# Kernel optimization log

Hardware: AMD Instinct MI355X
Metric: run time of the kernel (lower is better)

## Reference

```python
import jax, jax.numpy as jnp
import numpy as np

EPS_NORM = 1e-12   # F.normalize eps (denominator clamp)
EPS_PD = 1e-6      # F.pairwise_distance eps (added to the difference)
MARGIN = 0.3

B, D = 8192, 512


def setup_inputs() -> dict:
    key = jax.random.key(0)
    x = jax.random.normal(key, (B, D * 2), dtype=jnp.float32).reshape(B, 2, D)
    return {"x": x}


def reference(x):
    # x: [B, 2, D]  (anchor, positive)
    a = x[:, 0, :]
    p = x[:, 1, :]
    a = a / jnp.maximum(jnp.linalg.norm(a, axis=1, keepdims=True), EPS_NORM)
    p = p / jnp.maximum(jnp.linalg.norm(p, axis=1, keepdims=True), EPS_NORM)
    b, d = a.shape

    # output[i, j] = -||a_i - p_j + EPS_PD||^2, expanded so the BxB matrix
    # comes from one GEMM instead of a [B, D, B] broadcasted difference.
    sa2 = jnp.sum(a * a, axis=1)               # [B]
    sp2 = jnp.sum(p * p, axis=1)               # [B]
    dot = a @ p.T                              # [B, B]
    sa = jnp.sum(a, axis=1)                    # [B]
    sp = jnp.sum(p, axis=1)                    # [B]
    d2 = (sa2[:, None] + sp2[None, :] - 2.0 * dot
          + 2.0 * EPS_PD * (sa[:, None] - sp[None, :]) + d * (EPS_PD * EPS_PD))
    sim = -d2                                  # [B, B] similarity (detached in torch)

    # mineHardNegative with hard_rank=0, hard_prob=1: top-1 of descending sort
    # after removing the self index -> argmax over the row with diag masked.
    sim = jnp.where(jnp.eye(b, dtype=bool), -jnp.inf, sim)
    negidx = jnp.argmax(sim, axis=1)           # [B] int
    n = p[negidx]                              # hard negatives, [B, D]

    pos_d = jnp.linalg.norm(a - p + EPS_PD, axis=1)
    neg_d = jnp.linalg.norm(a - n + EPS_PD, axis=1)
    nloss = jnp.mean(jax.nn.relu(pos_d ** 2 - neg_d ** 2 + MARGIN))
    return nloss
```

## Files before the change

kernel.cpp:

```cpp
#include <hip/hip_runtime.h>
#include <stdint.h>
#include <math.h>

#define Bn 8192
#define Dn 512
#define EPSN 1e-12f
#define EPSP 1e-6f
#define MARG 0.3f

#define BM 128
#define BN 128
#define BKB 64
#define KT (Dn / BKB)
#define NCT (Bn / BN)
#define QS 256.0f
#define ISQ (2.0f / 65536.0f)

typedef int   int4v __attribute__((ext_vector_type(4)));
typedef float f32x4 __attribute__((ext_vector_type(4)));

__device__ __forceinline__ void async16(const void* g, void* l) {
    __builtin_amdgcn_global_load_lds(
        (const __attribute__((address_space(1))) void*)g,
        (__attribute__((address_space(3))) void*)l,
        16, 0, 0);
}

__device__ __forceinline__ unsigned long long packSI(float s, int idx) {
    union { float f; unsigned u; } c; c.f = s;
    const unsigned key = (c.u & 0x80000000u) ? ~c.u : (c.u | 0x80000000u);
    return ((unsigned long long)key << 32) | (unsigned)(~idx);
}
__device__ __forceinline__ float unpackS(unsigned long long p) {
    unsigned key = (unsigned)(p >> 32);
    union { unsigned u; float f; } c;
    c.u = (key & 0x80000000u) ? (key ^ 0x80000000u) : ~key;
    return c.f;
}

__global__ __launch_bounds__(256) void k_normalize(
    const float* __restrict__ x,
    uint8_t* __restrict__ a_i8, uint8_t* __restrict__ p_i8,
    float* __restrict__ cterm, float* __restrict__ rowconst,
    unsigned long long* __restrict__ rowmax)
{
    const int wave = threadIdx.x >> 6;
    const int lane = threadIdx.x & 63;
    const int i = blockIdx.x * 4 + wave;

    const float* srcA = x + (size_t)i * (2 * Dn) + lane * 8;
    const float* srcP = srcA + Dn;
    float4 a0 = ((const float4*)srcA)[0];
    float4 a1 = ((const float4*)srcA)[1];
    float4 p0 = ((const float4*)srcP)[0];
    float4 p1 = ((const float4*)srcP)[1];
    float va[8] = {a0.x, a0.y, a0.z, a0.w, a1.x, a1.y, a1.z, a1.w};
    float vp[8] = {p0.x, p0.y, p0.z, p0.w, p1.x, p1.y, p1.z, p1.w};

    float ssa = 0.f, ssp = 0.f;
#pragma unroll
    for (int j = 0; j < 8; ++j) { ssa += va[j] * va[j]; ssp += vp[j] * vp[j]; }
#pragma unroll
    for (int m = 1; m < 64; m <<= 1) {
        ssa += __shfl_xor(ssa, m);
        ssp += __shfl_xor(ssp, m);
    }
    const float sa = 1.0f / fmaxf(sqrtf(ssa), EPSN);
    const float sp = 1.0f / fmaxf(sqrtf(ssp), EPSN);

    float oa[8], op[8];
    float s1p = 0.f, s2p = 0.f, s1a = 0.f, s2a = 0.f, pos = 0.f;
#pragma unroll
    for (int j = 0; j < 8; ++j) {
        oa[j] = va[j] * sa;
        op[j] = vp[j] * sp;
        s1p += op[j]; s2p += op[j] * op[j];
        s1a += oa[j]; s2a += oa[j] * oa[j];
        const float u = oa[j] - op[j] + EPSP;
        pos += u * u;
    }

    uint64_t pka = 0, pkp = 0;
#pragma unroll
    for (int j = 0; j < 8; ++j) {
        int qa = (int)rintf(oa[j] * QS);
        int qp = (int)rintf(op[j] * QS);
        qa = qa > 127 ? 127 : (qa < -127 ? -127 : qa);
        qp = qp > 127 ? 127 : (qp < -127 ? -127 : qp);
        pka |= (uint64_t)(uint8_t)qa << (8 * j);
        pkp |= (uint64_t)(uint8_t)qp << (8 * j);
    }
    *(uint64_t*)(a_i8 + (size_t)i * Dn + lane * 8) = pka;
    *(uint64_t*)(p_i8 + (size_t)i * Dn + lane * 8) = pkp;

#pragma unroll
    for (int m = 1; m < 64; m <<= 1) {
        s1p += __shfl_xor(s1p, m);
        s2p += __shfl_xor(s2p, m);
        s1a += __shfl_xor(s1a, m);
        s2a += __shfl_xor(s2a, m);
        pos += __shfl_xor(pos, m);
    }
    if (lane == 0) {
        cterm[i] = -s2p + 2.0f * EPSP * s1p;
        rowconst[i] = pos - s2a - 2.0f * EPSP * s1a
                      - (float)Dn * EPSP * EPSP + MARG;
        rowmax[i] = 0ull;
    }
}

__global__ __launch_bounds__(256, 4) void k_gemm_argmax(
    const uint8_t* __restrict__ a_i8, const uint8_t* __restrict__ p_i8,
    const float* __restrict__ cterm,
    unsigned long long* __restrict__ rowmax)
{
    __shared__ uint8_t As[2][BM * BKB];
    __shared__ uint8_t Bs[2][BN * BKB];
    __shared__ unsigned long long rp[2][BM];

    const int t = threadIdx.x;
    const int wave = t >> 6;
    const int lane = t & 63;
    const int rowBase = blockIdx.y * BM;
    const int colBase = blockIdx.x * BN;

    const int q = lane >> 4;
    const int m16 = lane & 15;
    const int waveRow = (wave >> 1) * 64;
    const int waveCol = (wave & 1) * 64;

    const int r0 = t >> 2;
    const int g0 = (t & 3) ^ ((r0 >> 1) & 3);
    const int r1 = (256 + t) >> 2;
    const int g1 = ((256 + t) & 3) ^ ((r1 >> 1) & 3);
    const uint8_t* gA0 = a_i8 + (size_t)(rowBase + r0) * Dn + g0 * 16;
    const uint8_t* gA1 = a_i8 + (size_t)(rowBase + r1) * Dn + g1 * 16;
    const uint8_t* gB0 = p_i8 + (size_t)(colBase + r0) * Dn + g0 * 16;
    const uint8_t* gB1 = p_i8 + (size_t)(colBase + r1) * Dn + g1 * 16;
    const int ldsC0 = (wave * 64) * 16;
    const int ldsC1 = (256 + wave * 64) * 16;

    const int s0 = q ^ ((m16 >> 1) & 3);
    const int aBase = (waveRow + m16) * BKB + s0 * 16;
    const int bBase = (waveCol + m16) * BKB + s0 * 16;

    int4v acc[4][4];
#pragma unroll
    for (int a = 0; a < 4; ++a)
#pragma unroll
        for (int b = 0; b < 4; ++b) acc[a][b] = (int4v){0, 0, 0, 0};

    auto stage = [&](int buf, int ke) {
        async16(gA0 + ke, &As[buf][ldsC0]);
        async16(gA1 + ke, &As[buf][ldsC1]);
        async16(gB0 + ke, &Bs[buf][ldsC0]);
        async16(gB1 + ke, &Bs[buf][ldsC1]);
    };

    stage(0, 0);
#pragma unroll
    for (int kt = 0; kt < KT; ++kt) {
        const int cur = kt & 1;
        __syncthreads();
        if (kt + 1 < KT) stage(cur ^ 1, (kt + 1) * BKB);

        const uint8_t* pa = &As[cur][aBase];
        const uint8_t* pb = &Bs[cur][bBase];
        int4v af[4], bfr[4];
#pragma unroll
        for (int mt = 0; mt < 4; ++mt)
            af[mt] = *(const int4v*)(pa + mt * 16 * BKB);
#pragma unroll
        for (int nt = 0; nt < 4; ++nt)
            bfr[nt] = *(const int4v*)(pb + nt * 16 * BKB);
#pragma unroll
        for (int mt = 0; mt < 4; ++mt)
#pragma unroll
            for (int nt = 0; nt < 4; ++nt)
                acc[mt][nt] = __builtin_amdgcn_mfma_i32_16x16x64_i8(
                    af[mt], bfr[nt], acc[mt][nt], 0, 0, 0);
    }

    float cv[4];
#pragma unroll
    for (int nt = 0; nt < 4; ++nt)
        cv[nt] = cterm[colBase + waveCol + nt * 16 + m16];

#pragma unroll
    for (int mt = 0; mt < 4; ++mt) {
#pragma unroll
        for (int v = 0; v < 4; ++v) {
            const int lr = waveRow + mt * 16 + q * 4 + v;
            const int gi = rowBase + lr;
            unsigned long long best = 0;
#pragma unroll
            for (int nt = 0; nt < 4; ++nt) {
                const int gj = colBase + waveCol + nt * 16 + m16;
                float sc = ISQ * (float)acc[mt][nt][v] + cv[nt];
                unsigned long long pk = (gj == gi) ? 0ull : packSI(sc, gj);
                best = pk > best ? pk : best;
            }
#pragma unroll
            for (int msk = 1; msk < 16; msk <<= 1) {
                unsigned long long ob = __shfl_xor(best, msk);
                best = ob > best ? ob : best;
            }
            if (m16 == 0) rp[wave & 1][lr] = best;
        }
    }
    __syncthreads();
    if (t < BM) {
        unsigned long long b0 = rp[0][t];
        unsigned long long b1 = rp[1][t];
        if (b1 > b0) b0 = b1;
        atomicMax(&rowmax[rowBase + t], b0);
    }
}

__global__ __launch_bounds__(1024) void k_final(
    const unsigned long long* __restrict__ rowmax,
    const float* __restrict__ rowconst,
    float* __restrict__ out)
{
    __shared__ float sm[16];
    float s = 0.f;
    for (int k = threadIdx.x; k < Bn; k += 1024)
        s += fmaxf(rowconst[k] + unpackS(rowmax[k]), 0.f);
#pragma unroll
    for (int msk = 1; msk < 64; msk <<= 1) s += __shfl_xor(s, msk);
    if ((threadIdx.x & 63) == 0) sm[threadIdx.x >> 6] = s;
    __syncthreads();
    if (threadIdx.x == 0) {
        float tot = 0.f;
#pragma unroll
        for (int w = 0; w < 16; ++w) tot += sm[w];
        out[0] = tot * (1.0f / Bn);
    }
}

extern "C" void kernel_launch(void* const* d_in, const int* in_sizes, int n_in,
                              void* d_out, int out_size, void* d_ws, size_t ws_size,
                              hipStream_t stream)
{
    const float* x = (const float*)d_in[0];
    char* ws = (char*)d_ws;
    uint8_t*  a_i8     = (uint8_t*)(ws + 0);
    uint8_t*  p_i8     = (uint8_t*)(ws + 4194304);
    float*    cterm    = (float*)(ws + 8388608);
    float*    rowconst = (float*)(ws + 8421376);
    unsigned long long* rowmax =
        (unsigned long long*)(ws + 8454144);
    float*    out      = (float*)d_out;

    k_normalize<<<2048, 256, 0, stream>>>(x, a_i8, p_i8, cterm, rowconst, rowmax);
    k_gemm_argmax<<<dim3(NCT, Bn / BM), 256, 0, stream>>>(a_i8, p_i8, cterm, rowmax);
    k_final<<<1, 1024, 0, stream>>>(rowmax, rowconst, out);
}
```

Before: 137.0 us.

## Transpose GEMM operands so row max reduces in registers and drop packed index

```diff
diff --git a/kernel.cpp b/kernel.cpp
--- a/kernel.cpp
+++ b/kernel.cpp
@@ -26,15 +26,13 @@
         16, 0, 0);
 }
 
-__device__ __forceinline__ unsigned long long packSI(float s, int idx) {
+__device__ __forceinline__ unsigned key32(float s) {
     union { float f; unsigned u; } c; c.f = s;
-    const unsigned key = (c.u & 0x80000000u) ? ~c.u : (c.u | 0x80000000u);
-    return ((unsigned long long)key << 32) | (unsigned)(~idx);
-}
-__device__ __forceinline__ float unpackS(unsigned long long p) {
-    unsigned key = (unsigned)(p >> 32);
+    return (c.u & 0x80000000u) ? ~c.u : (c.u | 0x80000000u);
+}
+__device__ __forceinline__ float unkey32(unsigned k) {
     union { unsigned u; float f; } c;
-    c.u = (key & 0x80000000u) ? (key ^ 0x80000000u) : ~key;
+    c.u = (k & 0x80000000u) ? (k ^ 0x80000000u) : ~k;
     return c.f;
 }
 
@@ -42,7 +40,7 @@
     const float* __restrict__ x,
     uint8_t* __restrict__ a_i8, uint8_t* __restrict__ p_i8,
     float* __restrict__ cterm, float* __restrict__ rowconst,
-    unsigned long long* __restrict__ rowmax)
+    unsigned* __restrict__ rowmax)
 {
     const int wave = threadIdx.x >> 6;
     const int lane = threadIdx.x & 63;
@@ -105,18 +103,18 @@
         cterm[i] = -s2p + 2.0f * EPSP * s1p;
         rowconst[i] = pos - s2a - 2.0f * EPSP * s1a
                       - (float)Dn * EPSP * EPSP + MARG;
-        rowmax[i] = 0ull;
+        rowmax[i] = 0u;
     }
 }
 
 __global__ __launch_bounds__(256, 4) void k_gemm_argmax(
     const uint8_t* __restrict__ a_i8, const uint8_t* __restrict__ p_i8,
     const float* __restrict__ cterm,
-    unsigned long long* __restrict__ rowmax)
+    unsigned* __restrict__ rowmax)
 {
     __shared__ uint8_t As[2][BM * BKB];
     __shared__ uint8_t Bs[2][BN * BKB];
-    __shared__ unsigned long long rp[2][BM];
+    __shared__ unsigned sm[2][BN];
 
     const int t = threadIdx.x;
     const int wave = t >> 6;
@@ -133,10 +131,10 @@
     const int g0 = (t & 3) ^ ((r0 >> 1) & 3);
     const int r1 = (256 + t) >> 2;
     const int g1 = ((256 + t) & 3) ^ ((r1 >> 1) & 3);
-    const uint8_t* gA0 = a_i8 + (size_t)(rowBase + r0) * Dn + g0 * 16;
-    const uint8_t* gA1 = a_i8 + (size_t)(rowBase + r1) * Dn + g1 * 16;
-    const uint8_t* gB0 = p_i8 + (size_t)(colBase + r0) * Dn + g0 * 16;
-    const uint8_t* gB1 = p_i8 + (size_t)(colBase + r1) * Dn + g1 * 16;
+    const uint8_t* gA0 = p_i8 + (size_t)(rowBase + r0) * Dn + g0 * 16;
+    const uint8_t* gA1 = p_i8 + (size_t)(rowBase + r1) * Dn + g1 * 16;
+    const uint8_t* gB0 = a_i8 + (size_t)(colBase + r0) * Dn + g0 * 16;
+    const uint8_t* gB1 = a_i8 + (size_t)(colBase + r1) * Dn + g1 * 16;
     const int ldsC0 = (wave * 64) * 16;
     const int ldsC1 = (256 + wave * 64) * 16;
 
@@ -181,59 +179,78 @@
                     af[mt], bfr[nt], acc[mt][nt], 0, 0, 0);
     }
 
-    float cv[4];
-#pragma unroll
-    for (int nt = 0; nt < 4; ++nt)
-        cv[nt] = cterm[colBase + waveCol + nt * 16 + m16];
-
-#pragma unroll
-    for (int mt = 0; mt < 4; ++mt) {
-#pragma unroll
-        for (int v = 0; v < 4; ++v) {
-            const int lr = waveRow + mt * 16 + q * 4 + v;
-            const int gi = rowBase + lr;
-            unsigned long long best = 0;
-#pragma unroll
-            for (int nt = 0; nt < 4; ++nt) {
-                const int gj = colBase + waveCol + nt * 16 + m16;
-                float sc = ISQ * (float)acc[mt][nt][v] + cv[nt];
-                unsigned long long pk = (gj == gi) ? 0ull : packSI(sc, gj);
-                best = pk > best ? pk : best;
-            }
-#pragma unroll
-            for (int msk = 1; msk < 16; msk <<= 1) {
-                unsigned long long ob = __shfl_xor(best, msk);
-                best = ob > best ? ob : best;
-            }
-            if (m16 == 0) rp[wave & 1][lr] = best;
+    f32x4 cj[4];
+#pragma unroll
+    for (int mt = 0; mt < 4; ++mt)
+        cj[mt] = *(const f32x4*)(cterm + rowBase + waveRow + mt * 16 + q * 4);
+
+    unsigned kv[4];
+    const bool diag = (rowBase == colBase);
+    if (!diag) {
+#pragma unroll
+        for (int nt = 0; nt < 4; ++nt) {
+            float mx = -3.4e38f;
+#pragma unroll
+            for (int mt = 0; mt < 4; ++mt)
+#pragma unroll
+                for (int v = 0; v < 4; ++v)
+                    mx = fmaxf(mx, ISQ * (float)acc[mt][nt][v] + cj[mt][v]);
+            kv[nt] = key32(mx);
         }
+    } else {
+#pragma unroll
+        for (int nt = 0; nt < 4; ++nt) {
+            const int dtarget = waveCol - waveRow + nt * 16 + m16 - q * 4;
+            float mx = -3.4e38f;
+#pragma unroll
+            for (int mt = 0; mt < 4; ++mt)
+#pragma unroll
+                for (int v = 0; v < 4; ++v) {
+                    const float sc = ISQ * (float)acc[mt][nt][v] + cj[mt][v];
+                    mx = (mt * 16 + v == dtarget) ? mx : fmaxf(mx, sc);
+                }
+            kv[nt] = key32(mx);
+        }
+    }
+
+#pragma unroll
+    for (int nt = 0; nt < 4; ++nt) {
+#pragma unroll
+        for (int msk = 16; msk < 64; msk <<= 1) {
+            const unsigned o = (unsigned)__shfl_xor((int)kv[nt], msk);
+            kv[nt] = o > kv[nt] ? o : kv[nt];
+        }
+    }
+    if (lane < 16) {
+#pragma unroll
+        for (int nt = 0; nt < 4; ++nt)
+            sm[wave >> 1][(wave & 1) * 64 + nt * 16 + m16] = kv[nt];
     }
     __syncthreads();
-    if (t < BM) {
-        unsigned long long b0 = rp[0][t];
-        unsigned long long b1 = rp[1][t];
-        if (b1 > b0) b0 = b1;
-        atomicMax(&rowmax[rowBase + t], b0);
+    if (t < BN) {
+        const unsigned k0 = sm[0][t];
+        const unsigned k1 = sm[1][t];
+        atomicMax(&rowmax[colBase + t], k0 > k1 ? k0 : k1);
     }
 }
 
 __global__ __launch_bounds__(1024) void k_final(
-    const unsigned long long* __restrict__ rowmax,
+    const unsigned* __restrict__ rowmax,
     const float* __restrict__ rowconst,
     float* __restrict__ out)
 {
-    __shared__ float sm[16];
+    __shared__ float smf[16];
     float s = 0.f;
     for (int k = threadIdx.x; k < Bn; k += 1024)
-        s += fmaxf(rowconst[k] + unpackS(rowmax[k]), 0.f);
+        s += fmaxf(rowconst[k] + unkey32(rowmax[k]), 0.f);
 #pragma unroll
     for (int msk = 1; msk < 64; msk <<= 1) s += __shfl_xor(s, msk);
-    if ((threadIdx.x & 63) == 0) sm[threadIdx.x >> 6] = s;
+    if ((threadIdx.x & 63) == 0) smf[threadIdx.x >> 6] = s;
     __syncthreads();
     if (threadIdx.x == 0) {
         float tot = 0.f;
 #pragma unroll
-        for (int w = 0; w < 16; ++w) tot += sm[w];
+        for (int w = 0; w < 16; ++w) tot += smf[w];
         out[0] = tot * (1.0f / Bn);
     }
 }
@@ -248,8 +265,7 @@
     uint8_t*  p_i8     = (uint8_t*)(ws + 4194304);
     float*    cterm    = (float*)(ws + 8388608);
     float*    rowconst = (float*)(ws + 8421376);
-    unsigned long long* rowmax =
-        (unsigned long long*)(ws + 8454144);
+    unsigned* rowmax   = (unsigned*)(ws + 8454144);
     float*    out      = (float*)d_out;
 
     k_normalize<<<2048, 256, 0, stream>>>(x, a_i8, p_i8, cterm, rowconst, rowmax);
```

After: 117.7 us. 1.16x faster.
